# Optimization experiments

Hardware: AMD Instinct MI355X
Metric: run time of the kernel (lower is better)

The kernel has to match this reference:

```python
import jax, jax.numpy as jnp
import numpy as np

EMBED = 1024
HEADS = 16
HEAD_DIM = EMBED // HEADS


def setup_inputs() -> dict:
    key = jax.random.key(0)
    ks = jax.random.split(key, 6)
    N, S, E = 2, 2048, EMBED
    value = jax.random.normal(ks[0], (N, S, E), dtype=jnp.float32)
    k = jax.random.normal(ks[1], (N, S, E), dtype=jnp.float32)
    q = jax.random.normal(ks[2], (N, S, E), dtype=jnp.float32)
    mask = jax.random.randint(ks[3], (N, 1, S, S), 0, 2, dtype=jnp.int32)
    W_fc = jax.random.normal(ks[4], (E, E), dtype=jnp.float32) * (1.0 / np.sqrt(E))
    b_fc = jax.random.normal(ks[5], (E,), dtype=jnp.float32) * 0.01
    return {"value": value, "key": k, "query": q, "mask": mask, "W_fc": W_fc, "b_fc": b_fc}


def reference(value, key, query, mask, W_fc, b_fc):
    N, Sq, E = query.shape
    Sk = key.shape[1]
    Sv = value.shape[1]
    # NOTE: the original module never applies its q/k/v Linear layers (source bug);
    # it only reshapes into heads.
    v = value.reshape(N, Sv, HEADS, HEAD_DIM)
    k = key.reshape(N, Sk, HEADS, HEAD_DIM)
    q = query.reshape(N, Sq, HEADS, HEAD_DIM)
    # energy: [N, H, Q, K]
    energy = jnp.einsum('nqhd,nkhd->nhqk', q, k)
    energy = jnp.where(mask == 0, jnp.float32(-1e20), energy)
    # scale by sqrt(embed_size) as in the source (not sqrt(head_dim))
    attention = jax.nn.softmax(energy / jnp.sqrt(jnp.float32(E)), axis=3)
    out = jnp.einsum('nhql,nlhd->nqhd', attention, v).reshape(N, Sq, E)
    # torch Linear: x @ W.T + b
    out = out @ W_fc.T + b_fc
    return out
```

## Files before the change

kernel.cpp:

```cpp
#include <hip/hip_runtime.h>
#include <hip/hip_bf16.h>
#include <math.h>

#define S_LEN 2048
#define EMB   1024
#define HEADS 16
#define HDIM  64
#define SPLIT 4

#define C_SCALE   0.045084439f
#define BIAS_OK  -2.0f

#define NE  ((size_t)2 * S_LEN * EMB)
#define NL  ((size_t)2 * S_LEN * HEADS)
#define NMB ((size_t)2 * S_LEN * S_LEN / 64)

typedef __bf16 bf16x8 __attribute__((ext_vector_type(8)));
typedef float  f32x4  __attribute__((ext_vector_type(4)));
typedef float  f32x16 __attribute__((ext_vector_type(16)));

__device__ __forceinline__ bf16x8 cvt8(const float* v) {
    bf16x8 r;
#pragma unroll
    for (int i = 0; i < 8; ++i) r[i] = (__bf16)v[i];
    return r;
}
__device__ __forceinline__ unsigned long long pack4(float a, float b, float c, float d) {
    __bf16 t[4] = {(__bf16)a, (__bf16)b, (__bf16)c, (__bf16)d};
    return *(unsigned long long*)t;
}
__device__ __forceinline__ bf16x8 cat2(unsigned long long lo, unsigned long long hi) {
    unsigned long long t[2] = {lo, hi};
    return *(bf16x8*)t;
}
__device__ __forceinline__ void gld_lds16(const void* g, void* l) {
    __builtin_amdgcn_global_load_lds(
        (const __attribute__((address_space(1))) void*)g,
        (__attribute__((address_space(3))) void*)l, 16, 0, 0);
}

__global__ __launch_bounds__(256)
void prepass_kernel(const float* __restrict__ Wf, const int* __restrict__ Mp,
                    __bf16* __restrict__ Wb, unsigned long long* __restrict__ Mb) {
    const int bid = blockIdx.x, tid = threadIdx.x;
    if (bid < 512) {
        size_t i = ((size_t)bid * 256 + tid) * 8;
        float t[8];
        *(float4*)&t[0] = *(const float4*)(Wf + i);
        *(float4*)&t[4] = *(const float4*)(Wf + i + 4);
        *(bf16x8*)(Wb + i) = cvt8(t);
    } else {
        const int w = tid >> 6, lane = tid & 63;
        const int wg = (bid - 512) * 4 + w;
#pragma unroll 4
        for (int it = 0; it < 64; ++it) {
            size_t W = (size_t)wg * 64 + it;
            int v = Mp[W * 64 + lane];
            unsigned long long b = __ballot(v != 0);
            if (lane == 0) Mb[W] = b;
        }
    }
}

__global__ __launch_bounds__(256, 4)
void attn_kernel(const float* __restrict__ Vp, const float* __restrict__ Kp,
                 const float* __restrict__ Qp, const unsigned long long* __restrict__ Mb,
                 __bf16* __restrict__ Opart, float* __restrict__ Lpart) {
    __shared__ __bf16 Klds[64 * 64];
    __shared__ __bf16 Vtlds[64 * 64];

    const int tid  = threadIdx.x;
    const int lane = tid & 63;
    const int w    = tid >> 6;
    const int nblk = 2 * HEADS * SPLIT * 16;
    const int bid  = (blockIdx.x & 7) * (nblk / 8) + (blockIdx.x >> 3);
    const int qt = bid & 15;
    const int sp = (bid >> 4) & (SPLIT - 1);
    const int h  = (bid >> 6) & 15;
    const int n  = bid >> 10;

    const int ql = lane & 31;
    const int g  = lane >> 5;

    const float* qbase = Qp + (size_t)n * S_LEN * EMB + h * HDIM;
    const float* kbase = Kp + (size_t)n * S_LEN * EMB + h * HDIM;
    const float* vbase = Vp + (size_t)n * S_LEN * EMB + h * HDIM;

    const int q = qt * 128 + w * 32 + ql;

    bf16x8 qfrag[4];
#pragma unroll
    for (int ds_ = 0; ds_ < 4; ++ds_) {
        const float* qp = qbase + (size_t)q * EMB + ds_ * 16 + g * 8;
        float tmp[8];
        *(float4*)&tmp[0] = *(const float4*)qp;
        *(float4*)&tmp[4] = *(const float4*)(qp + 4);
        qfrag[ds_] = cvt8(tmp);
    }

    f32x16 oacc[2] = {};
    float la = 0.f;

    const unsigned long long* mrow = Mb + ((size_t)(n * S_LEN + q) << 5);

    const int sk  = tid >> 2;
    const int sdq = (tid & 3) * 16;
    const int d0  = (tid & 31) * 2;
    const int kv8 = (tid >> 5) * 8;

    const int kvbase = sp * (S_LEN / SPLIT);
    const int niter  = (S_LEN / SPLIT) / 64;

#pragma unroll 1
    for (int t = 0; t < niter; ++t) {
        const int kv0 = kvbase + t * 64;
        __syncthreads();
        {
            const float* kp = kbase + (size_t)(kv0 + sk) * EMB + sdq;
            float tk[16];
            *(float4*)&tk[0]  = *(const float4*)kp;
            *(float4*)&tk[4]  = *(const float4*)(kp + 4);
            *(float4*)&tk[8]  = *(const float4*)(kp + 8);
            *(float4*)&tk[12] = *(const float4*)(kp + 12);
            *(bf16x8*)((char*)Klds + sk * 128 + ((sdq * 2)       ^ ((sk & 7) << 4))) = cvt8(&tk[0]);
            *(bf16x8*)((char*)Klds + sk * 128 + (((sdq + 8) * 2) ^ ((sk & 7) << 4))) = cvt8(&tk[8]);

            const float* vp = vbase + (size_t)(kv0 + kv8) * EMB + d0;
            float r0[8], r1[8];
#pragma unroll
            for (int j = 0; j < 8; ++j) {
                float2 tv = *(const float2*)(vp + (size_t)j * EMB);
                r0[j] = tv.x; r1[j] = tv.y;
            }
            *(bf16x8*)((char*)Vtlds + d0 * 128       + ((kv8 * 2) ^ ((d0 & 7) << 4)))       = cvt8(r0);
            *(bf16x8*)((char*)Vtlds + (d0 + 1) * 128 + ((kv8 * 2) ^ (((d0 + 1) & 7) << 4))) = cvt8(r1);
        }
        __syncthreads();

        const unsigned long long m64 = mrow[kv0 >> 6];

#pragma unroll
        for (int kt = 0; kt < 2; ++kt) {
            f32x16 E = {};
            __builtin_amdgcn_s_setprio(1);
#pragma unroll
            for (int ds_ = 0; ds_ < 4; ++ds_) {
                int row = kt * 32 + ql;
                bf16x8 kf = *(const bf16x8*)((char*)Klds + row * 128 +
                    ((ds_ * 32 + g * 16) ^ ((row & 7) << 4)));
                E = __builtin_amdgcn_mfma_f32_32x32x16_bf16(kf, qfrag[ds_], E, 0, 0, 0);
            }
            __builtin_amdgcn_s_setprio(0);

            const unsigned u = (unsigned)(m64 >> (kt * 32 + 4 * g));
            unsigned long long own[4];
#pragma unroll
            for (int rq = 0; rq < 4; ++rq) {
                unsigned nib = u >> (8 * rq);
                float p0 = __builtin_amdgcn_exp2f(fmaf(E[4*rq+0], C_SCALE, BIAS_OK)) * (float)(nib & 1u);
                float p1 = __builtin_amdgcn_exp2f(fmaf(E[4*rq+1], C_SCALE, BIAS_OK)) * (float)((nib >> 1) & 1u);
                float p2 = __builtin_amdgcn_exp2f(fmaf(E[4*rq+2], C_SCALE, BIAS_OK)) * (float)((nib >> 2) & 1u);
                float p3 = __builtin_amdgcn_exp2f(fmaf(E[4*rq+3], C_SCALE, BIAS_OK)) * (float)((nib >> 3) & 1u);
                la += (p0 + p1) + (p2 + p3);
                own[rq] = pack4(p0, p1, p2, p3);
            }

            unsigned long long sa = g ? own[0] : own[1];
            unsigned long long sb = g ? own[2] : own[3];
            unsigned long long ra = __shfl_xor((long long)sa, 32);
            unsigned long long rb = __shfl_xor((long long)sb, 32);
            bf16x8 frag0 = g ? cat2(ra, own[1]) : cat2(own[0], ra);
            bf16x8 frag1 = g ? cat2(rb, own[3]) : cat2(own[2], rb);

            __builtin_amdgcn_s_setprio(1);
#pragma unroll
            for (int dt = 0; dt < 2; ++dt) {
                int row = dt * 32 + ql;
                bf16x8 v0 = *(const bf16x8*)((char*)Vtlds + row * 128 +
                    (((2*kt) * 32 + g * 16) ^ ((row & 7) << 4)));
                bf16x8 v1 = *(const bf16x8*)((char*)Vtlds + row * 128 +
                    (((2*kt+1) * 32 + g * 16) ^ ((row & 7) << 4)));
                oacc[dt] = __builtin_amdgcn_mfma_f32_32x32x16_bf16(v0, frag0, oacc[dt], 0, 0, 0);
                oacc[dt] = __builtin_amdgcn_mfma_f32_32x32x16_bf16(v1, frag1, oacc[dt], 0, 0, 0);
            }
            __builtin_amdgcn_s_setprio(0);
        }
    }

    float lt = la + __shfl_xor(la, 32);
    __bf16* op = Opart + (size_t)sp * NE + ((size_t)n * S_LEN + q) * EMB + h * HDIM;
#pragma unroll
    for (int dt = 0; dt < 2; ++dt)
#pragma unroll
        for (int rq = 0; rq < 4; ++rq)
            *(unsigned long long*)(op + dt * 32 + 8 * rq + 4 * g) =
                pack4(oacc[dt][4*rq], oacc[dt][4*rq+1], oacc[dt][4*rq+2], oacc[dt][4*rq+3]);
    if (g == 0)
        Lpart[(size_t)sp * NL + ((size_t)n * S_LEN + q) * HEADS + h] = lt;
}

__global__ __launch_bounds__(256)
void reduce_kernel(const __bf16* __restrict__ Opart, const float* __restrict__ Lpart,
                   __bf16* __restrict__ X) {
    size_t e0 = ((size_t)blockIdx.x * 256 + threadIdx.x) * 8;
    size_t hr = e0 >> 6;
    float l = 0.f;
#pragma unroll
    for (int s = 0; s < SPLIT; ++s) l += Lpart[s * NL + hr];
    float inv = 1.f / l;
    float acc[8] = {};
#pragma unroll
    for (int s = 0; s < SPLIT; ++s) {
        bf16x8 v = *(const bf16x8*)(Opart + s * NE + e0);
#pragma unroll
        for (int i = 0; i < 8; ++i) acc[i] += (float)v[i];
    }
    bf16x8 r;
#pragma unroll
    for (int i = 0; i < 8; ++i) r[i] = (__bf16)(acc[i] * inv);
    *(bf16x8*)(X + e0) = r;
}

__global__ __launch_bounds__(256)
void fc_kernel(const __bf16* __restrict__ X, const __bf16* __restrict__ Wb,
               const float* __restrict__ bfc, float* __restrict__ Out) {
    __shared__ __bf16 Al[128 * 32];
    __shared__ __bf16 Bl[128 * 32];
    const int tid = threadIdx.x, lane = tid & 63, w = tid >> 6;
    const int ql = lane & 15, g = lane >> 4;
    const int bm = blockIdx.x >> 3, bn = blockIdx.x & 7;
    const int wr = w >> 1, wc = w & 1;

    const int rowL = lane >> 2;
    const int colE = (lane & 3) * 8;

    f32x4 acc[4][4] = {};

    for (int k0 = 0; k0 < EMB; k0 += 32) {
        __syncthreads();
        const int q0 = w * 2, q1 = w * 2 + 1;
        gld_lds16(X  + (size_t)(bm * 128 + q0 * 16 + rowL) * EMB + k0 + colE, Al + q0 * 512);
        gld_lds16(X  + (size_t)(bm * 128 + q1 * 16 + rowL) * EMB + k0 + colE, Al + q1 * 512);
        gld_lds16(Wb + (size_t)(bn * 128 + q0 * 16 + rowL) * EMB + k0 + colE, Bl + q0 * 512);
        gld_lds16(Wb + (size_t)(bn * 128 + q1 * 16 + rowL) * EMB + k0 + colE, Bl + q1 * 512);
        __syncthreads();

        bf16x8 a[4], b[4];
#pragma unroll
        for (int mi = 0; mi < 4; ++mi)
            a[mi] = *(const bf16x8*)(Al + (wr * 64 + mi * 16 + ql) * 32 + g * 8);
#pragma unroll
        for (int nj = 0; nj < 4; ++nj)
            b[nj] = *(const bf16x8*)(Bl + (wc * 64 + nj * 16 + ql) * 32 + g * 8);
#pragma unroll
        for (int mi = 0; mi < 4; ++mi)
#pragma unroll
            for (int nj = 0; nj < 4; ++nj)
                acc[mi][nj] = __builtin_amdgcn_mfma_f32_16x16x32_bf16(a[mi], b[nj], acc[mi][nj], 0, 0, 0);
    }

#pragma unroll
    for (int nj = 0; nj < 4; ++nj) {
        int col = bn * 128 + wc * 64 + nj * 16 + ql;
        float bias = bfc[col];
#pragma unroll
        for (int mi = 0; mi < 4; ++mi) {
            int row0 = bm * 128 + wr * 64 + mi * 16 + g * 4;
#pragma unroll
            for (int r = 0; r < 4; ++r)
                Out[(size_t)(row0 + r) * EMB + col] = acc[mi][nj][r] + bias;
        }
    }
}

extern "C" void kernel_launch(void* const* d_in, const int* in_sizes, int n_in,
                              void* d_out, int out_size, void* d_ws, size_t ws_size,
                              hipStream_t stream) {
    const float* Vp = (const float*)d_in[0];
    const float* Kp = (const float*)d_in[1];
    const float* Qp = (const float*)d_in[2];
    const int*   Mp = (const int*)d_in[3];
    const float* Wf = (const float*)d_in[4];
    const float* bf = (const float*)d_in[5];
    float* Out = (float*)d_out;

    char* p = (char*)d_ws;
    __bf16* Opart = (__bf16*)p;             p += SPLIT * NE * 2;
    float*  Lpart = (float*)p;              p += SPLIT * NL * 4;
    __bf16* Wb    = (__bf16*)p;             p += (size_t)EMB * EMB * 2;
    unsigned long long* Mb = (unsigned long long*)p;

    prepass_kernel<<<dim3(1024), dim3(256), 0, stream>>>(Wf, Mp, Wb, Mb);
    attn_kernel<<<dim3(2 * HEADS * SPLIT * 16), dim3(256), 0, stream>>>(Vp, Kp, Qp, Mb, Opart, Lpart);
    reduce_kernel<<<dim3(NE / 8 / 256), dim3(256), 0, stream>>>(Opart, Lpart, Opart);
    fc_kernel<<<dim3((2 * S_LEN / 128) * (EMB / 128)), dim3(256), 0, stream>>>(Opart, Wb, bf, Out);
}
```

Measured before the change: 131.3 us.

## Double-buffer K/V tiles in LDS with register prefetch of next tile

Doubles the K and V^T LDS buffers and prefetches the next 64-row K/V tile from global memory into registers before computing on the current tile. The converted tile is written into the other buffer after compute, which cuts the loop from two barriers to one. The goal is to hide global load latency behind the MFMA and softmax work. The cost is 32 extra float registers per thread and double the LDS (32KB per block), which may reduce occupancy at launch_bounds(256,4).

Measured after the change: 175.4 us. 1.34x slower.

```diff
diff --git a/kernel.cpp b/kernel.cpp
--- a/kernel.cpp
+++ b/kernel.cpp
@@ -7,6 +7,7 @@
 #define HEADS 16
 #define HDIM  64
 #define SPLIT 4
+#define NITER ((S_LEN / SPLIT) / 64)
 
 #define C_SCALE   0.045084439f
 #define BIAS_OK  -2.0f
@@ -66,8 +67,8 @@
 void attn_kernel(const float* __restrict__ Vp, const float* __restrict__ Kp,
                  const float* __restrict__ Qp, const unsigned long long* __restrict__ Mb,
                  __bf16* __restrict__ Opart, float* __restrict__ Lpart) {
-    __shared__ __bf16 Klds[64 * 64];
-    __shared__ __bf16 Vtlds[64 * 64];
+    __shared__ __bf16 Klds[2][64 * 64];
+    __shared__ __bf16 Vtlds[2][64 * 64];
 
     const int tid  = threadIdx.x;
     const int lane = tid & 63;
@@ -101,7 +102,7 @@
     f32x16 oacc[2] = {};
     float la = 0.f;
 
-    const unsigned long long* mrow = Mb + ((size_t)(n * S_LEN + q) << 5);
+    const unsigned long long* mrow = Mb + ((size_t)(n * S_LEN + q) << 5) + sp * NITER;
 
     const int sk  = tid >> 2;
     const int sdq = (tid & 3) * 16;
@@ -109,35 +110,40 @@
     const int kv8 = (tid >> 5) * 8;
 
     const int kvbase = sp * (S_LEN / SPLIT);
-    const int niter  = (S_LEN / SPLIT) / 64;
+
+    float kreg[16], vreg[16];
+
+#define LOADKV(T) do {                                                                \
+        const float* kp_ = kbase + (size_t)(kvbase + (T) * 64 + sk) * EMB + sdq;      \
+        *(float4*)&kreg[0]  = *(const float4*)kp_;                                    \
+        *(float4*)&kreg[4]  = *(const float4*)(kp_ + 4);                              \
+        *(float4*)&kreg[8]  = *(const float4*)(kp_ + 8);                              \
+        *(float4*)&kreg[12] = *(const float4*)(kp_ + 12);                             \
+        const float* vp_ = vbase + (size_t)(kvbase + (T) * 64 + kv8) * EMB + d0;      \
+        _Pragma("unroll")                                                             \
+        for (int j = 0; j < 8; ++j)                                                   \
+            *(float2*)&vreg[j * 2] = *(const float2*)(vp_ + (size_t)j * EMB);         \
+    } while (0)
+
+#define WRITEKV(B) do {                                                               \
+        *(bf16x8*)((char*)Klds[B] + sk * 128 + ((sdq * 2)       ^ ((sk & 7) << 4))) = cvt8(&kreg[0]); \
+        *(bf16x8*)((char*)Klds[B] + sk * 128 + (((sdq + 8) * 2) ^ ((sk & 7) << 4))) = cvt8(&kreg[8]); \
+        float r0_[8], r1_[8];                                                         \
+        _Pragma("unroll")                                                             \
+        for (int j = 0; j < 8; ++j) { r0_[j] = vreg[2 * j]; r1_[j] = vreg[2 * j + 1]; } \
+        *(bf16x8*)((char*)Vtlds[B] + d0 * 128       + ((kv8 * 2) ^ ((d0 & 7) << 4)))       = cvt8(r0_); \
+        *(bf16x8*)((char*)Vtlds[B] + (d0 + 1) * 128 + ((kv8 * 2) ^ (((d0 + 1) & 7) << 4))) = cvt8(r1_); \
+    } while (0)
+
+    LOADKV(0);
+    WRITEKV(0);
+    __syncthreads();
 
 #pragma unroll 1
-    for (int t = 0; t < niter; ++t) {
-        const int kv0 = kvbase + t * 64;
-        __syncthreads();
-        {
-            const float* kp = kbase + (size_t)(kv0 + sk) * EMB + sdq;
-            float tk[16];
-            *(float4*)&tk[0]  = *(const float4*)kp;
-            *(float4*)&tk[4]  = *(const float4*)(kp + 4);
-            *(float4*)&tk[8]  = *(const float4*)(kp + 8);
-            *(float4*)&tk[12] = *(const float4*)(kp + 12);
-            *(bf16x8*)((char*)Klds + sk * 128 + ((sdq * 2)       ^ ((sk & 7) << 4))) = cvt8(&tk[0]);
-            *(bf16x8*)((char*)Klds + sk * 128 + (((sdq + 8) * 2) ^ ((sk & 7) << 4))) = cvt8(&tk[8]);
-
-            const float* vp = vbase + (size_t)(kv0 + kv8) * EMB + d0;
-            float r0[8], r1[8];
-#pragma unroll
-            for (int j = 0; j < 8; ++j) {
-                float2 tv = *(const float2*)(vp + (size_t)j * EMB);
-                r0[j] = tv.x; r1[j] = tv.y;
-            }
-            *(bf16x8*)((char*)Vtlds + d0 * 128       + ((kv8 * 2) ^ ((d0 & 7) << 4)))       = cvt8(r0);
-            *(bf16x8*)((char*)Vtlds + (d0 + 1) * 128 + ((kv8 * 2) ^ (((d0 + 1) & 7) << 4))) = cvt8(r1);
-        }
-        __syncthreads();
-
-        const unsigned long long m64 = mrow[kv0 >> 6];
+    for (int t = 0; t < NITER; ++t) {
+        const int buf = t & 1;
+        if (t < NITER - 1) LOADKV(t + 1);
+        const unsigned long long m64 = mrow[t];
 
 #pragma unroll
         for (int kt = 0; kt < 2; ++kt) {
@@ -146,7 +152,7 @@
 #pragma unroll
             for (int ds_ = 0; ds_ < 4; ++ds_) {
                 int row = kt * 32 + ql;
-                bf16x8 kf = *(const bf16x8*)((char*)Klds + row * 128 +
+                bf16x8 kf = *(const bf16x8*)((char*)Klds[buf] + row * 128 +
                     ((ds_ * 32 + g * 16) ^ ((row & 7) << 4)));
                 E = __builtin_amdgcn_mfma_f32_32x32x16_bf16(kf, qfrag[ds_], E, 0, 0, 0);
             }
@@ -176,16 +182,21 @@
 #pragma unroll
             for (int dt = 0; dt < 2; ++dt) {
                 int row = dt * 32 + ql;
-                bf16x8 v0 = *(const bf16x8*)((char*)Vtlds + row * 128 +
+                bf16x8 v0 = *(const bf16x8*)((char*)Vtlds[buf] + row * 128 +
                     (((2*kt) * 32 + g * 16) ^ ((row & 7) << 4)));
-                bf16x8 v1 = *(const bf16x8*)((char*)Vtlds + row * 128 +
+                bf16x8 v1 = *(const bf16x8*)((char*)Vtlds[buf] + row * 128 +
                     (((2*kt+1) * 32 + g * 16) ^ ((row & 7) << 4)));
                 oacc[dt] = __builtin_amdgcn_mfma_f32_32x32x16_bf16(v0, frag0, oacc[dt], 0, 0, 0);
                 oacc[dt] = __builtin_amdgcn_mfma_f32_32x32x16_bf16(v1, frag1, oacc[dt], 0, 0, 0);
             }
             __builtin_amdgcn_s_setprio(0);
         }
-    }
+
+        if (t < NITER - 1) WRITEKV(buf ^ 1);
+        __syncthreads();
+    }
+#undef LOADKV
+#undef WRITEKV
 
     float lt = la + __shfl_xor(la, 32);
     __bf16* op = Opart + (size_t)sp * NE + ((size_t)n * S_LEN + q) * EMB + h * HDIM;
```
